# Kernel tuning notes

Measured on AMD Instinct MI355X. Metric: run time of the kernel, lower is better.

The kernel has to match this reference:

```python
import jax, jax.numpy as jnp
import numpy as np

B, N, K = 4096, 87, 87


def setup_inputs() -> dict:
    key = jax.random.key(0)
    ks = jax.random.split(key, 6)
    x = jax.random.normal(ks[0], (B, N, N), dtype=jnp.float32)
    evals = jax.random.uniform(ks[1], (B, K), dtype=jnp.float32)
    evecs = jax.random.normal(ks[2], (B, N, K), dtype=jnp.float32)
    # learned per-node diffusion times (torch inits to 0, clamped to 1e-8;
    # use small positive values to exercise the exp decay)
    diffusion_time = jax.random.uniform(ks[3], (N,), dtype=jnp.float32) * 0.1
    # MiniMLP: single Linear(2*N -> N)
    lim = 1.0 / np.sqrt(2 * N)
    W = jax.random.uniform(ks[4], (N, 2 * N), minval=-lim, maxval=lim, dtype=jnp.float32)
    b = jax.random.uniform(ks[5], (N,), minval=-lim, maxval=lim, dtype=jnp.float32)
    return {"x": x, "evals": evals, "evecs": evecs,
            "diffusion_time": diffusion_time, "W": W, "b": b}


def reference(x, evals, evecs, diffusion_time, W, b):
    # clamp diffusion times (torch does this in-place on .data)
    t = jnp.maximum(diffusion_time, 1e-8)                     # (N,)
    # expa[b,i,m] = exp(-t_i * eval[b,m])
    expa = jnp.exp(-t[None, :, None] * evals[:, None, :])     # (B,N,K)
    # kernel[b,i,j] = sum_m evec[b,i,m] * expa[b,i,m] * evec[b,j,m]
    # (equivalent to the diag_embed + triple matmul + diagonal in the torch code)
    kernel = jnp.einsum('bim,bjm->bij', evecs * expa, evecs)  # (B,N,N)
    x_diffuse = jnp.concatenate([x, kernel], axis=2)          # (B,N,2N)
    return x_diffuse @ W.T + b                                # (B,N,N)
```

## Files before the change

kernel.cpp:

```cpp
#include <hip/hip_runtime.h>
#include <hip/hip_bf16.h>
#include <math.h>

#define NN    87
#define NN2   (NN * NN)
#define EPW   92
#define EFN   8012
#define XSN   8020
#define WPH   104
#define WPANEL (96 * WPH)
#define NT    256

#define WS_W     0
#define WS_EPAD  (2 * WPANEL * 2)
#define EPAD_N   8360
#define WS_NEED  (WS_EPAD + EPAD_N * 4)

typedef __attribute__((ext_vector_type(8))) short bf16x8;
typedef __attribute__((ext_vector_type(4))) short bf16x4;
typedef __attribute__((ext_vector_type(4))) float f32x4;
typedef float f32x4u __attribute__((ext_vector_type(4), aligned(4)));

__device__ __forceinline__ short f2bf(float f) {
    __hip_bfloat16 h = __float2bfloat16(f);
    return *(short*)&h;
}

__device__ __forceinline__ void gl16(const float* g, float* l) {
    __builtin_amdgcn_global_load_lds(
        (const __attribute__((address_space(1))) void*)g,
        (__attribute__((address_space(3))) void*)l, 16, 0, 0);
}

__global__ void prep(const float* __restrict__ W, const float* __restrict__ evecs,
                     int B, char* __restrict__ ws)
{
    int idx = (int)blockIdx.x * NT + (int)threadIdx.x;
    short* wp = (short*)(ws + WS_W);
    float* ep = (float*)(ws + WS_EPAD);
    if (idx < 2 * WPANEL) {
        int p = idx / WPANEL, rem = idx - p * WPANEL;
        int r = rem / WPH, c = rem - r * WPH;
        short v = 0;
        if (r < NN && c < NN) v = f2bf(W[r * (2 * NN) + p * NN + c]);
        wp[idx] = v;
    }
    int i2 = idx - 2 * WPANEL;
    if (i2 >= 0 && i2 < EPAD_N)
        ep[i2] = (i2 < NN2) ? evecs[(size_t)(B - 1) * NN2 + i2] : 0.f;
}

template <bool WS>
__device__ __forceinline__ bf16x8 wload(const short* __restrict__ wp,
                                        const float* __restrict__ gW,
                                        int panel, int jrow, int jcl, int k0, bool tailKs)
{
    if constexpr (WS) {
        return *(const bf16x8*)&wp[panel * WPANEL + jrow * WPH + k0];
    } else {
        float v[8];
        if (!tailKs) {
            f32x4u a  = *(const f32x4u*)(gW + jcl * (2 * NN) + panel * NN + k0);
            f32x4u b4 = *(const f32x4u*)(gW + jcl * (2 * NN) + panel * NN + k0 + 4);
            v[0] = a.x; v[1] = a.y; v[2] = a.z; v[3] = a.w;
            v[4] = b4.x; v[5] = b4.y; v[6] = b4.z; v[7] = b4.w;
        } else {
            #pragma unroll
            for (int q = 0; q < 8; ++q) {
                int k = k0 + q;
                v[q] = (k < NN) ? gW[jcl * (2 * NN) + panel * NN + k] : 0.f;
            }
        }
        bf16x8 o;
        #pragma unroll
        for (int q = 0; q < 8; ++q) o[q] = f2bf(v[q]);
        return o;
    }
}

template <bool WS>
__global__ __launch_bounds__(NT, 4)
void fused(const float* __restrict__ gx, const float* __restrict__ gevals,
           const float* __restrict__ gevecs, const float* __restrict__ dtime,
           const float* __restrict__ gW, const float* __restrict__ bias,
           const char* __restrict__ ws, int B, float* __restrict__ out)
{
    __shared__ __align__(16) float sE[EFN];
    __shared__ __align__(16) short sX[XSN];
    __shared__ float sLam[96];
    short* const sD = (short*)sE;

    const int b    = (int)blockIdx.x;
    const int tid  = (int)threadIdx.x;
    const int lane = tid & 63;
    const int wave = tid >> 6;
    const int l15  = lane & 15;
    const int lk   = lane >> 4;
    const int i0   = (wave >> 1) * 48;
    const int j0   = (wave & 1) * 48;

    const float* __restrict__ Eb = gevecs + (size_t)b * NN2;
    const float* __restrict__ xb = gx     + (size_t)b * NN2;
    const short* wp = nullptr;
    if constexpr (WS) {
        wp = (const short*)(ws + WS_W);
        if (b == B - 1) Eb = (const float*)(ws + WS_EPAD);
    }

    if (tid < 96) sLam[tid] = (tid < NN) ? gevals[(size_t)b * NN + tid] : 3e38f;

    int iw[3], jw[3], iru[3], jru[3];
    float tr_[3];
    #pragma unroll
    for (int r = 0; r < 3; ++r) {
        iw[r]  = i0 + 16 * r + l15;
        jw[r]  = j0 + 16 * r + l15;
        iru[r] = (iw[r] < NN) ? iw[r] : NN - 1;
        jru[r] = (jw[r] < NN) ? jw[r] : NN - 1;
        tr_[r] = fmaxf(dtime[iru[r]], 1e-8f);
    }

    if (tid < 8) sE[NN * EPW + tid] = 0.f;

    if constexpr (WS) {
        for (int vc = wave; vc < 32; vc += 4) {
            int p   = vc * 256 + lane * 4;
            int row = p / EPW;
            int col = p - row * EPW;
            const float* g = Eb + row * NN + col;
            if (vc < 31) gl16(g, &sE[vc * 256]);
            else if (lane < 17) gl16(g, &sE[vc * 256]);
        }
    } else {
        for (int u = tid; u < NN * 22; u += NT) {
            int r = u / 22, sg = u - r * 22, c = sg * 4;
            const float* pE = Eb + r * NN + c;
            if (sg < 21) *(f32x4*)&sE[r * EPW + c] = *(const f32x4u*)pE;
            else { f32x4 t; t.x = pE[0]; t.y = pE[1]; t.z = pE[2]; t.w = 0.f;
                   *(f32x4*)&sE[r * EPW + c] = t; }
        }
        for (int u = tid; u < NN * 4; u += NT) {
            int r = u >> 2, c = 88 + (u & 3);
            sE[r * EPW + c] = 0.f;
        }
    }

    float xq[8][4];
    float x7568 = 0.f;
    #pragma unroll
    for (int k = 0; k < 8; ++k) {
        int u = tid + k * NT;
        int uc = (u < 1892) ? u : 1891;
        f32x4u t = *(const f32x4u*)(xb + 4 * uc);
        xq[k][0] = t.x; xq[k][1] = t.y; xq[k][2] = t.z; xq[k][3] = t.w;
    }
    if (tid == 0) x7568 = xb[7568];

    if constexpr (WS) {
        asm volatile("s_waitcnt vmcnt(8) lgkmcnt(0)" ::: "memory");
        __builtin_amdgcn_s_barrier();
        __builtin_amdgcn_sched_barrier(0);
    } else {
        __syncthreads();
    }

    f32x4 acc1[3][3];
    #pragma unroll
    for (int c = 0; c < 3; ++c)
        #pragma unroll
        for (int r = 0; r < 3; ++r) acc1[c][r] = (f32x4){0.f, 0.f, 0.f, 0.f};

    #pragma unroll
    for (int ks = 0; ks < 3; ++ks) {
        const int k0 = ks * 32 + lk * 8;
        f32x4 la  = *(const f32x4*)&sLam[k0];
        f32x4 lb4 = *(const f32x4*)&sLam[k0 + 4];
        float l8_[8] = {la.x, la.y, la.z, la.w, lb4.x, lb4.y, lb4.z, lb4.w};

        bf16x8 ef[3], af[3];
        #pragma unroll
        for (int c = 0; c < 3; ++c) {
            f32x4 lo = *(const f32x4*)&sE[jru[c] * EPW + k0];
            f32x4 hi = *(const f32x4*)&sE[jru[c] * EPW + k0 + 4];
            #pragma unroll
            for (int q = 0; q < 4; ++q) { ef[c][q] = f2bf(lo[q]); ef[c][q + 4] = f2bf(hi[q]); }
        }
        #pragma unroll
        for (int r = 0; r < 3; ++r) {
            f32x4 lo = *(const f32x4*)&sE[iru[r] * EPW + k0];
            f32x4 hi = *(const f32x4*)&sE[iru[r] * EPW + k0 + 4];
            #pragma unroll
            for (int q = 0; q < 4; ++q) {
                af[r][q]     = f2bf(lo[q] * __expf(-tr_[r] * l8_[q]));
                af[r][q + 4] = f2bf(hi[q] * __expf(-tr_[r] * l8_[q + 4]));
            }
        }
        #pragma unroll
        for (int c = 0; c < 3; ++c)
            #pragma unroll
            for (int r = 0; r < 3; ++r)
                acc1[c][r] = __builtin_amdgcn_mfma_f32_16x16x32_bf16(ef[c], af[r], acc1[c][r], 0, 0, 0);
    }
    __syncthreads();

    #pragma unroll
    for (int c = 0; c < 3; ++c) {
        const int jb = j0 + 16 * c + lk * 4;
        if (jb < EPW) {
            #pragma unroll
            for (int r = 0; r < 3; ++r) {
                if (iw[r] < NN) {
                    bf16x4 v = {f2bf(acc1[c][r][0]), f2bf(acc1[c][r][1]),
                                f2bf(acc1[c][r][2]), f2bf(acc1[c][r][3])};
                    *(bf16x4*)&sD[iw[r] * EPW + jb] = v;
                }
            }
        }
    }
    if (tid < 4) sD[NN * EPW + tid] = 0;
    __builtin_amdgcn_sched_barrier(0);

    #pragma unroll
    for (int k = 0; k < 8; ++k) {
        int u = tid + k * NT;
        if (u < 1892) {
            int f = 4 * u;
            #pragma unroll
            for (int e = 0; e < 4; ++e) {
                int fe = f + e;
                if (fe < NN2) {
                    int r = fe / NN, c = fe - r * NN;
                    sX[r * EPW + c] = f2bf(xq[k][e]);
                }
            }
        }
    }
    if (tid == 0) sX[86 * EPW + 86] = f2bf(x7568);
    for (int u = tid; u < NN * 5; u += NT) {
        int r = u / 5, c = NN + u % 5;
        sX[r * EPW + c] = 0;
    }
    if (tid < 16) sX[NN * EPW + tid] = 0;

    bf16x8 wfx[3][3];
    float bjv[3][4];
    #pragma unroll
    for (int ks = 0; ks < 3; ++ks)
        #pragma unroll
        for (int wr = 0; wr < 3; ++wr)
            wfx[ks][wr] = wload<WS>(wp, gW, 0, jw[wr], jru[wr], ks * 32 + lk * 8, ks == 2);
    #pragma unroll
    for (int wr = 0; wr < 3; ++wr) {
        const int jb = j0 + 16 * wr + lk * 4;
        if (jb + 3 < NN) {
            f32x4u t = *(const f32x4u*)(bias + jb);
            bjv[wr][0] = t.x; bjv[wr][1] = t.y; bjv[wr][2] = t.z; bjv[wr][3] = t.w;
        } else {
            #pragma unroll
            for (int q = 0; q < 4; ++q) bjv[wr][q] = (jb + q < NN) ? bias[jb + q] : 0.f;
        }
    }
    __syncthreads();

    f32x4 acc2[3][3];
    #pragma unroll
    for (int wr = 0; wr < 3; ++wr)
        #pragma unroll
        for (int xc = 0; xc < 3; ++xc) {
            acc2[wr][xc][0] = bjv[wr][0]; acc2[wr][xc][1] = bjv[wr][1];
            acc2[wr][xc][2] = bjv[wr][2]; acc2[wr][xc][3] = bjv[wr][3];
        }

    #pragma unroll
    for (int ks = 0; ks < 3; ++ks) {
        const int k0 = ks * 32 + lk * 8;
        bf16x8 xf[3];
        #pragma unroll
        for (int xc = 0; xc < 3; ++xc) {
            bf16x4 lo = *(const bf16x4*)&sX[iru[xc] * EPW + k0];
            bf16x4 hi = *(const bf16x4*)&sX[iru[xc] * EPW + k0 + 4];
            #pragma unroll
            for (int q = 0; q < 4; ++q) { xf[xc][q] = lo[q]; xf[xc][q + 4] = hi[q]; }
        }
        #pragma unroll
        for (int wr = 0; wr < 3; ++wr)
            #pragma unroll
            for (int xc = 0; xc < 3; ++xc)
                acc2[wr][xc] = __builtin_amdgcn_mfma_f32_16x16x32_bf16(wfx[ks][wr], xf[xc], acc2[wr][xc], 0, 0, 0);
    }
    #pragma unroll
    for (int ks = 0; ks < 3; ++ks) {
        const int k0 = ks * 32 + lk * 8;
        bf16x8 wfd[3], df[3];
        #pragma unroll
        for (int wr = 0; wr < 3; ++wr)
            wfd[wr] = wload<WS>(wp, gW, 1, jw[wr], jru[wr], k0, ks == 2);
        #pragma unroll
        for (int xc = 0; xc < 3; ++xc) {
            bf16x4 lo = *(const bf16x4*)&sD[iru[xc] * EPW + k0];
            bf16x4 hi = *(const bf16x4*)&sD[iru[xc] * EPW + k0 + 4];
            #pragma unroll
            for (int q = 0; q < 4; ++q) { df[xc][q] = lo[q]; df[xc][q + 4] = hi[q]; }
        }
        #pragma unroll
        for (int wr = 0; wr < 3; ++wr)
            #pragma unroll
            for (int xc = 0; xc < 3; ++xc)
                acc2[wr][xc] = __builtin_amdgcn_mfma_f32_16x16x32_bf16(wfd[wr], df[xc], acc2[wr][xc], 0, 0, 0);
    }

    {
        float* __restrict__ gb = out + (size_t)b * NN2;
        #pragma unroll
        for (int wr = 0; wr < 3; ++wr) {
            const int jb = j0 + 16 * wr + lk * 4;
            #pragma unroll
            for (int xc = 0; xc < 3; ++xc) {
                const int i = iw[xc];
                if (i < NN) {
                    if (jb + 3 < NN) {
                        f32x4u v;
                        v.x = acc2[wr][xc][0]; v.y = acc2[wr][xc][1];
                        v.z = acc2[wr][xc][2]; v.w = acc2[wr][xc][3];
                        *(f32x4u*)&gb[i * NN + jb] = v;
                    } else {
                        #pragma unroll
                        for (int q = 0; q < 4; ++q)
                            if (jb + q < NN) gb[i * NN + jb + q] = acc2[wr][xc][q];
                    }
                }
            }
        }
    }
}

extern "C" void kernel_launch(void* const* d_in, const int* in_sizes, int n_in,
                              void* d_out, int out_size, void* d_ws, size_t ws_size,
                              hipStream_t stream)
{
    const float* x     = (const float*)d_in[0];
    const float* evals = (const float*)d_in[1];
    const float* evecs = (const float*)d_in[2];
    const float* dtime = (const float*)d_in[3];
    const float* W     = (const float*)d_in[4];
    const float* bias  = (const float*)d_in[5];
    float* out = (float*)d_out;

    const int B = in_sizes[1] / NN;

    if (ws_size >= (size_t)WS_NEED) {
        const int prep_elems = 2 * WPANEL + EPAD_N;
        prep<<<(prep_elems + NT - 1) / NT, NT, 0, stream>>>(W, evecs, B, (char*)d_ws);
        fused<true><<<dim3(B), dim3(NT), 0, stream>>>(x, evals, evecs, dtime, W, bias,
                                                      (const char*)d_ws, B, out);
    } else {
        fused<false><<<dim3(B), dim3(NT), 0, stream>>>(x, evals, evecs, dtime, W, bias,
                                                       nullptr, B, out);
    }
}
```

Baseline: 96.33 us.

## Make fused kernel persistent and prefetch next batch's evecs during GEMM

Switches to a persistent grid of 768 blocks that loop over batches. While each batch's output GEMM runs, the next batch's evecs are staged into shared memory and its evals are prefetched into a double-buffered array. x is now read straight from global into registers instead of going through shared memory, W fragments are loaded once per iteration, and occupancy drops to 3 blocks per CU. This aims to hide load latency and cut launch and per-block setup costs, at the risk of higher register pressure and less parallelism from the smaller grid.

Result: slower. 158.8 us (+64.9%).

```diff
diff --git a/kernel.cpp b/kernel.cpp
--- a/kernel.cpp
+++ b/kernel.cpp
@@ -5,16 +5,18 @@
 #define NN    87
 #define NN2   (NN * NN)
 #define EPW   92
-#define EFN   8012
-#define XSN   8020
+#define EFN   (NN * EPW + 8)
+#define SDN   (NN * EPW + 4)
 #define WPH   104
 #define WPANEL (96 * WPH)
 #define NT    256
-
+#define GRIDB 768
+
+#define PAD_N    8360
 #define WS_W     0
 #define WS_EPAD  (2 * WPANEL * 2)
-#define EPAD_N   8360
-#define WS_NEED  (WS_EPAD + EPAD_N * 4)
+#define WS_XPAD  (WS_EPAD + PAD_N * 4)
+#define WS_NEED  (WS_XPAD + PAD_N * 4)
 
 typedef __attribute__((ext_vector_type(8))) short bf16x8;
 typedef __attribute__((ext_vector_type(4))) short bf16x4;
@@ -33,21 +35,23 @@
 }
 
 __global__ void prep(const float* __restrict__ W, const float* __restrict__ evecs,
-                     int B, char* __restrict__ ws)
+                     const float* __restrict__ x, int B, char* __restrict__ ws)
 {
     int idx = (int)blockIdx.x * NT + (int)threadIdx.x;
-    short* wp = (short*)(ws + WS_W);
-    float* ep = (float*)(ws + WS_EPAD);
+    short* wpp = (short*)(ws + WS_W);
+    float* ep  = (float*)(ws + WS_EPAD);
+    float* xp  = (float*)(ws + WS_XPAD);
     if (idx < 2 * WPANEL) {
         int p = idx / WPANEL, rem = idx - p * WPANEL;
         int r = rem / WPH, c = rem - r * WPH;
         short v = 0;
         if (r < NN && c < NN) v = f2bf(W[r * (2 * NN) + p * NN + c]);
-        wp[idx] = v;
+        wpp[idx] = v;
     }
     int i2 = idx - 2 * WPANEL;
-    if (i2 >= 0 && i2 < EPAD_N)
-        ep[i2] = (i2 < NN2) ? evecs[(size_t)(B - 1) * NN2 + i2] : 0.f;
+    if (i2 >= 0 && i2 < PAD_N) ep[i2] = (i2 < NN2) ? evecs[(size_t)(B - 1) * NN2 + i2] : 0.f;
+    int i3 = i2 - PAD_N;
+    if (i3 >= 0 && i3 < PAD_N) xp[i3] = (i3 < NN2) ? x[(size_t)(B - 1) * NN2 + i3] : 0.f;
 }
 
 template <bool WS>
@@ -79,18 +83,44 @@
 }
 
 template <bool WS>
-__global__ __launch_bounds__(NT, 4)
+__device__ __forceinline__ void stageE(const float* __restrict__ Eb, float* __restrict__ sE,
+                                       int tid, int wave, int lane)
+{
+    if constexpr (WS) {
+        for (int vc = wave; vc < 32; vc += 4) {
+            int p   = vc * 256 + lane * 4;
+            int row = p / EPW;
+            int col = p - row * EPW;
+            const float* g = Eb + row * NN + col;
+            if (vc < 31) gl16(g, &sE[vc * 256]);
+            else if (lane < 17) gl16(g, &sE[vc * 256]);
+        }
+    } else {
+        for (int u = tid; u < NN * 22; u += NT) {
+            int r = u / 22, sg = u - r * 22, c = sg * 4;
+            const float* pE = Eb + r * NN + c;
+            if (sg < 21) *(f32x4*)&sE[r * EPW + c] = *(const f32x4u*)pE;
+            else { f32x4 t; t.x = pE[0]; t.y = pE[1]; t.z = pE[2]; t.w = 0.f;
+                   *(f32x4*)&sE[r * EPW + c] = t; }
+        }
+        for (int u = tid; u < NN * 4; u += NT) {
+            int r = u >> 2, c = 88 + (u & 3);
+            sE[r * EPW + c] = 0.f;
+        }
+    }
+}
+
+template <bool WS>
+__global__ __launch_bounds__(NT, 3)
 void fused(const float* __restrict__ gx, const float* __restrict__ gevals,
            const float* __restrict__ gevecs, const float* __restrict__ dtime,
            const float* __restrict__ gW, const float* __restrict__ bias,
-           const char* __restrict__ ws, int B, float* __restrict__ out)
+           const char* __restrict__ ws, int B, int gridB, float* __restrict__ out)
 {
     __shared__ __align__(16) float sE[EFN];
-    __shared__ __align__(16) short sX[XSN];
-    __shared__ float sLam[96];
-    short* const sD = (short*)sE;
-
-    const int b    = (int)blockIdx.x;
+    __shared__ __align__(16) short sD[SDN];
+    __shared__ float sLam[2][96];
+
     const int tid  = (int)threadIdx.x;
     const int lane = tid & 63;
     const int wave = tid >> 6;
@@ -99,15 +129,14 @@
     const int i0   = (wave >> 1) * 48;
     const int j0   = (wave & 1) * 48;
 
-    const float* __restrict__ Eb = gevecs + (size_t)b * NN2;
-    const float* __restrict__ xb = gx     + (size_t)b * NN2;
-    const short* wp = nullptr;
+    const short* wp   = nullptr;
+    const float* epad = nullptr;
+    const float* xpad = nullptr;
     if constexpr (WS) {
-        wp = (const short*)(ws + WS_W);
-        if (b == B - 1) Eb = (const float*)(ws + WS_EPAD);
-    }
-
-    if (tid < 96) sLam[tid] = (tid < NN) ? gevals[(size_t)b * NN + tid] : 3e38f;
+        wp   = (const short*)(ws + WS_W);
+        epad = (const float*)(ws + WS_EPAD);
+        xpad = (const float*)(ws + WS_XPAD);
+    }
 
     int iw[3], jw[3], iru[3], jru[3];
     float tr_[3];
@@ -120,135 +149,7 @@
         tr_[r] = fmaxf(dtime[iru[r]], 1e-8f);
     }
 
-    if (tid < 8) sE[NN * EPW + tid] = 0.f;
-
-    if constexpr (WS) {
-        for (int vc = wave; vc < 32; vc += 4) {
-            int p   = vc * 256 + lane * 4;
-            int row = p / EPW;
-            int col = p - row * EPW;
-            const float* g = Eb + row * NN + col;
-            if (vc < 31) gl16(g, &sE[vc * 256]);
-            else if (lane < 17) gl16(g, &sE[vc * 256]);
-        }
-    } else {
-        for (int u = tid; u < NN * 22; u += NT) {
-            int r = u / 22, sg = u - r * 22, c = sg * 4;
-            const float* pE = Eb + r * NN + c;
-            if (sg < 21) *(f32x4*)&sE[r * EPW + c] = *(const f32x4u*)pE;
-            else { f32x4 t; t.x = pE[0]; t.y = pE[1]; t.z = pE[2]; t.w = 0.f;
-                   *(f32x4*)&sE[r * EPW + c] = t; }
-        }
-        for (int u = tid; u < NN * 4; u += NT) {
-            int r = u >> 2, c = 88 + (u & 3);
-            sE[r * EPW + c] = 0.f;
-        }
-    }
-
-    float xq[8][4];
-    float x7568 = 0.f;
-    #pragma unroll
-    for (int k = 0; k < 8; ++k) {
-        int u = tid + k * NT;
-        int uc = (u < 1892) ? u : 1891;
-        f32x4u t = *(const f32x4u*)(xb + 4 * uc);
-        xq[k][0] = t.x; xq[k][1] = t.y; xq[k][2] = t.z; xq[k][3] = t.w;
-    }
-    if (tid == 0) x7568 = xb[7568];
-
-    if constexpr (WS) {
-        asm volatile("s_waitcnt vmcnt(8) lgkmcnt(0)" ::: "memory");
-        __builtin_amdgcn_s_barrier();
-        __builtin_amdgcn_sched_barrier(0);
-    } else {
-        __syncthreads();
-    }
-
-    f32x4 acc1[3][3];
-    #pragma unroll
-    for (int c = 0; c < 3; ++c)
-        #pragma unroll
-        for (int r = 0; r < 3; ++r) acc1[c][r] = (f32x4){0.f, 0.f, 0.f, 0.f};
-
-    #pragma unroll
-    for (int ks = 0; ks < 3; ++ks) {
-        const int k0 = ks * 32 + lk * 8;
-        f32x4 la  = *(const f32x4*)&sLam[k0];
-        f32x4 lb4 = *(const f32x4*)&sLam[k0 + 4];
-        float l8_[8] = {la.x, la.y, la.z, la.w, lb4.x, lb4.y, lb4.z, lb4.w};
-
-        bf16x8 ef[3], af[3];
-        #pragma unroll
-        for (int c = 0; c < 3; ++c) {
-            f32x4 lo = *(const f32x4*)&sE[jru[c] * EPW + k0];
-            f32x4 hi = *(const f32x4*)&sE[jru[c] * EPW + k0 + 4];
-            #pragma unroll
-            for (int q = 0; q < 4; ++q) { ef[c][q] = f2bf(lo[q]); ef[c][q + 4] = f2bf(hi[q]); }
-        }
-        #pragma unroll
-        for (int r = 0; r < 3; ++r) {
-            f32x4 lo = *(const f32x4*)&sE[iru[r] * EPW + k0];
-            f32x4 hi = *(const f32x4*)&sE[iru[r] * EPW + k0 + 4];
-            #pragma unroll
-            for (int q = 0; q < 4; ++q) {
-                af[r][q]     = f2bf(lo[q] * __expf(-tr_[r] * l8_[q]));
-                af[r][q + 4] = f2bf(hi[q] * __expf(-tr_[r] * l8_[q + 4]));
-            }
-        }
-        #pragma unroll
-        for (int c = 0; c < 3; ++c)
-            #pragma unroll
-            for (int r = 0; r < 3; ++r)
-                acc1[c][r] = __builtin_amdgcn_mfma_f32_16x16x32_bf16(ef[c], af[r], acc1[c][r], 0, 0, 0);
-    }
-    __syncthreads();
-
-    #pragma unroll
-    for (int c = 0; c < 3; ++c) {
-        const int jb = j0 + 16 * c + lk * 4;
-        if (jb < EPW) {
-            #pragma unroll
-            for (int r = 0; r < 3; ++r) {
-                if (iw[r] < NN) {
-                    bf16x4 v = {f2bf(acc1[c][r][0]), f2bf(acc1[c][r][1]),
-                                f2bf(acc1[c][r][2]), f2bf(acc1[c][r][3])};
-                    *(bf16x4*)&sD[iw[r] * EPW + jb] = v;
-                }
-            }
-        }
-    }
-    if (tid < 4) sD[NN * EPW + tid] = 0;
-    __builtin_amdgcn_sched_barrier(0);
-
-    #pragma unroll
-    for (int k = 0; k < 8; ++k) {
-        int u = tid + k * NT;
-        if (u < 1892) {
-            int f = 4 * u;
-            #pragma unroll
-            for (int e = 0; e < 4; ++e) {
-                int fe = f + e;
-                if (fe < NN2) {
-                    int r = fe / NN, c = fe - r * NN;
-                    sX[r * EPW + c] = f2bf(xq[k][e]);
-                }
-            }
-        }
-    }
-    if (tid == 0) sX[86 * EPW + 86] = f2bf(x7568);
-    for (int u = tid; u < NN * 5; u += NT) {
-        int r = u / 5, c = NN + u % 5;
-        sX[r * EPW + c] = 0;
-    }
-    if (tid < 16) sX[NN * EPW + tid] = 0;
-
-    bf16x8 wfx[3][3];
     float bjv[3][4];
-    #pragma unroll
-    for (int ks = 0; ks < 3; ++ks)
-        #pragma unroll
-        for (int wr = 0; wr < 3; ++wr)
-            wfx[ks][wr] = wload<WS>(wp, gW, 0, jw[wr], jru[wr], ks * 32 + lk * 8, ks == 2);
     #pragma unroll
     for (int wr = 0; wr < 3; ++wr) {
         const int jb = j0 + 16 * wr + lk * 4;
@@ -260,77 +161,201 @@
             for (int q = 0; q < 4; ++q) bjv[wr][q] = (jb + q < NN) ? bias[jb + q] : 0.f;
         }
     }
+
+    if (tid < 8) sE[NN * EPW + tid] = 0.f;
+    if (tid < 4) sD[NN * EPW + tid] = 0;
+
+    const int b0 = (int)blockIdx.x;
+    {
+        const float* Eb = gevecs + (size_t)b0 * NN2;
+        if (WS && b0 == B - 1) Eb = epad;
+        float lamv = 3e38f;
+        if (tid < NN) lamv = gevals[(size_t)b0 * NN + tid];
+        stageE<WS>(Eb, sE, tid, wave, lane);
+        if (tid < 96) sLam[0][tid] = (tid < NN) ? lamv : 3e38f;
+    }
     __syncthreads();
 
-    f32x4 acc2[3][3];
-    #pragma unroll
-    for (int wr = 0; wr < 3; ++wr)
-        #pragma unroll
-        for (int xc = 0; xc < 3; ++xc) {
-            acc2[wr][xc][0] = bjv[wr][0]; acc2[wr][xc][1] = bjv[wr][1];
-            acc2[wr][xc][2] = bjv[wr][2]; acc2[wr][xc][3] = bjv[wr][3];
-        }
-
-    #pragma unroll
-    for (int ks = 0; ks < 3; ++ks) {
-        const int k0 = ks * 32 + lk * 8;
-        bf16x8 xf[3];
-        #pragma unroll
-        for (int xc = 0; xc < 3; ++xc) {
-            bf16x4 lo = *(const bf16x4*)&sX[iru[xc] * EPW + k0];
-            bf16x4 hi = *(const bf16x4*)&sX[iru[xc] * EPW + k0 + 4];
-            #pragma unroll
-            for (int q = 0; q < 4; ++q) { xf[xc][q] = lo[q]; xf[xc][q + 4] = hi[q]; }
-        }
-        #pragma unroll
-        for (int wr = 0; wr < 3; ++wr)
-            #pragma unroll
-            for (int xc = 0; xc < 3; ++xc)
-                acc2[wr][xc] = __builtin_amdgcn_mfma_f32_16x16x32_bf16(wfx[ks][wr], xf[xc], acc2[wr][xc], 0, 0, 0);
-    }
-    #pragma unroll
-    for (int ks = 0; ks < 3; ++ks) {
-        const int k0 = ks * 32 + lk * 8;
-        bf16x8 wfd[3], df[3];
-        #pragma unroll
-        for (int wr = 0; wr < 3; ++wr)
-            wfd[wr] = wload<WS>(wp, gW, 1, jw[wr], jru[wr], k0, ks == 2);
-        #pragma unroll
-        for (int xc = 0; xc < 3; ++xc) {
-            bf16x4 lo = *(const bf16x4*)&sD[iru[xc] * EPW + k0];
-            bf16x4 hi = *(const bf16x4*)&sD[iru[xc] * EPW + k0 + 4];
-            #pragma unroll
-            for (int q = 0; q < 4; ++q) { df[xc][q] = lo[q]; df[xc][q + 4] = hi[q]; }
-        }
-        #pragma unroll
-        for (int wr = 0; wr < 3; ++wr)
-            #pragma unroll
-            for (int xc = 0; xc < 3; ++xc)
-                acc2[wr][xc] = __builtin_amdgcn_mfma_f32_16x16x32_bf16(wfd[wr], df[xc], acc2[wr][xc], 0, 0, 0);
-    }
-
-    {
-        float* __restrict__ gb = out + (size_t)b * NN2;
-        #pragma unroll
-        for (int wr = 0; wr < 3; ++wr) {
-            const int jb = j0 + 16 * wr + lk * 4;
-            #pragma unroll
-            for (int xc = 0; xc < 3; ++xc) {
-                const int i = iw[xc];
-                if (i < NN) {
-                    if (jb + 3 < NN) {
-                        f32x4u v;
-                        v.x = acc2[wr][xc][0]; v.y = acc2[wr][xc][1];
-                        v.z = acc2[wr][xc][2]; v.w = acc2[wr][xc][3];
-                        *(f32x4u*)&gb[i * NN + jb] = v;
-                    } else {
-                        #pragma unroll
-                        for (int q = 0; q < 4; ++q)
-                            if (jb + q < NN) gb[i * NN + jb + q] = acc2[wr][xc][q];
+    for (int it = 0, b = b0; b < B; ++it, b += gridB) {
+        const int  bn = b + gridB;
+        const bool hn = bn < B;
+        const int  lbuf = it & 1;
+
+        f32x4 acc1[3][3];
+        #pragma unroll
+        for (int c = 0; c < 3; ++c)
+            #pragma unroll
+            for (int r = 0; r < 3; ++r) acc1[c][r] = (f32x4){0.f, 0.f, 0.f, 0.f};
+
+        #pragma unroll
+        for (int ks = 0; ks < 3; ++ks) {
+            const int k0 = ks * 32 + lk * 8;
+            f32x4 la  = *(const f32x4*)&sLam[lbuf][k0];
+            f32x4 lb4 = *(const f32x4*)&sLam[lbuf][k0 + 4];
+            float l8_[8] = {la.x, la.y, la.z, la.w, lb4.x, lb4.y, lb4.z, lb4.w};
+
+            bf16x8 ef[3], af[3];
+            #pragma unroll
+            for (int c = 0; c < 3; ++c) {
+                f32x4 lo = *(const f32x4*)&sE[jru[c] * EPW + k0];
+                f32x4 hi = *(const f32x4*)&sE[jru[c] * EPW + k0 + 4];
+                #pragma unroll
+                for (int q = 0; q < 4; ++q) { ef[c][q] = f2bf(lo[q]); ef[c][q + 4] = f2bf(hi[q]); }
+            }
+            #pragma unroll
+            for (int r = 0; r < 3; ++r) {
+                f32x4 lo = *(const f32x4*)&sE[iru[r] * EPW + k0];
+                f32x4 hi = *(const f32x4*)&sE[iru[r] * EPW + k0 + 4];
+                #pragma unroll
+                for (int q = 0; q < 4; ++q) {
+                    af[r][q]     = f2bf(lo[q] * __expf(-tr_[r] * l8_[q]));
+                    af[r][q + 4] = f2bf(hi[q] * __expf(-tr_[r] * l8_[q + 4]));
+                }
+            }
+            #pragma unroll
+            for (int c = 0; c < 3; ++c)
+                #pragma unroll
+                for (int r = 0; r < 3; ++r)
+                    acc1[c][r] = __builtin_amdgcn_mfma_f32_16x16x32_bf16(ef[c], af[r], acc1[c][r], 0, 0, 0);
+        }
+        __syncthreads();
+
+        #pragma unroll
+        for (int c = 0; c < 3; ++c) {
+            const int jb = j0 + 16 * c + lk * 4;
+            if (jb < EPW) {
+                #pragma unroll
+                for (int r = 0; r < 3; ++r) {
+                    if (iw[r] < NN) {
+                        bf16x4 v = {f2bf(acc1[c][r][0]), f2bf(acc1[c][r][1]),
+                                    f2bf(acc1[c][r][2]), f2bf(acc1[c][r][3])};
+                        *(bf16x4*)&sD[iw[r] * EPW + jb] = v;
                     }
                 }
             }
         }
+
+        bf16x8 wfx[3][3], wfd[3][3];
+        #pragma unroll
+        for (int ks = 0; ks < 3; ++ks)
+            #pragma unroll
+            for (int wr = 0; wr < 3; ++wr) {
+                wfx[ks][wr] = wload<WS>(wp, gW, 0, jw[wr], jru[wr], ks * 32 + lk * 8, ks == 2);
+                wfd[ks][wr] = wload<WS>(wp, gW, 1, jw[wr], jru[wr], ks * 32 + lk * 8, ks == 2);
+            }
+        float lamn = 3e38f;
+        if (hn && tid < NN) lamn = gevals[(size_t)bn * NN + tid];
+
+        const float* xbb = gx + (size_t)b * NN2;
+        bool xvec = true;
+        if (b == B - 1) { if (WS) xbb = xpad; else xvec = false; }
+        float xr[3][3][8];
+        #pragma unroll
+        for (int xc = 0; xc < 3; ++xc)
+            #pragma unroll
+            for (int ks = 0; ks < 3; ++ks) {
+                const int off = iru[xc] * NN + ks * 32 + lk * 8;
+                if (xvec) {
+                    f32x4u a  = *(const f32x4u*)(xbb + off);
+                    f32x4u b4 = *(const f32x4u*)(xbb + off + 4);
+                    xr[xc][ks][0] = a.x;  xr[xc][ks][1] = a.y;
+                    xr[xc][ks][2] = a.z;  xr[xc][ks][3] = a.w;
+                    xr[xc][ks][4] = b4.x; xr[xc][ks][5] = b4.y;
+                    xr[xc][ks][6] = b4.z; xr[xc][ks][7] = b4.w;
+                } else {
+                    #pragma unroll
+                    for (int q = 0; q < 8; ++q) {
+                        int o = off + q;
+                        xr[xc][ks][q] = xbb[(o < NN2) ? o : (NN2 - 1)];
+                    }
+                }
+            }
+
+        __builtin_amdgcn_sched_barrier(0);
+
+        if (hn) {
+            const float* Ebn = gevecs + (size_t)bn * NN2;
+            if (WS && bn == B - 1) Ebn = epad;
+            stageE<WS>(Ebn, sE, tid, wave, lane);
+        }
+
+        asm volatile("s_waitcnt lgkmcnt(0)" ::: "memory");
+        __builtin_amdgcn_s_barrier();
+        __builtin_amdgcn_sched_barrier(0);
+
+        bf16x8 xf[3][3];
+        #pragma unroll
+        for (int xc = 0; xc < 3; ++xc)
+            #pragma unroll
+            for (int ks = 0; ks < 3; ++ks)
+                #pragma unroll
+                for (int q = 0; q < 8; ++q)
+                    xf[xc][ks][q] = f2bf(xr[xc][ks][q]);
+
+        f32x4 acc2[3][3];
+        #pragma unroll
+        for (int wr = 0; wr < 3; ++wr)
+            #pragma unroll
+            for (int xc = 0; xc < 3; ++xc) {
+                acc2[wr][xc][0] = bjv[wr][0]; acc2[wr][xc][1] = bjv[wr][1];
+                acc2[wr][xc][2] = bjv[wr][2]; acc2[wr][xc][3] = bjv[wr][3];
+            }
+
+        #pragma unroll
+        for (int ks = 0; ks < 3; ++ks)
+            #pragma unroll
+            for (int wr = 0; wr < 3; ++wr)
+                #pragma unroll
+                for (int xc = 0; xc < 3; ++xc)
+                    acc2[wr][xc] = __builtin_amdgcn_mfma_f32_16x16x32_bf16(
+                        wfx[ks][wr], xf[xc][ks], acc2[wr][xc], 0, 0, 0);
+
+        #pragma unroll
+        for (int ks = 0; ks < 3; ++ks) {
+            const int k0 = ks * 32 + lk * 8;
+            bf16x8 df[3];
+            #pragma unroll
+            for (int xc = 0; xc < 3; ++xc) {
+                bf16x4 lo = *(const bf16x4*)&sD[iru[xc] * EPW + k0];
+                bf16x4 hi = *(const bf16x4*)&sD[iru[xc] * EPW + k0 + 4];
+                #pragma unroll
+                for (int q = 0; q < 4; ++q) { df[xc][q] = lo[q]; df[xc][q + 4] = hi[q]; }
+            }
+            #pragma unroll
+            for (int wr = 0; wr < 3; ++wr)
+                #pragma unroll
+                for (int xc = 0; xc < 3; ++xc)
+                    acc2[wr][xc] = __builtin_amdgcn_mfma_f32_16x16x32_bf16(
+                        wfd[ks][wr], df[xc], acc2[wr][xc], 0, 0, 0);
+        }
+
+        if (hn && tid < 96) sLam[(it + 1) & 1][tid] = (tid < NN) ? lamn : 3e38f;
+
+        {
+            float* __restrict__ gb = out + (size_t)b * NN2;
+            #pragma unroll
+            for (int wr = 0; wr < 3; ++wr) {
+                const int jb = j0 + 16 * wr + lk * 4;
+                #pragma unroll
+                for (int xc = 0; xc < 3; ++xc) {
+                    const int i = iw[xc];
+                    if (i < NN) {
+                        if (jb + 3 < NN) {
+                            f32x4u v;
+                            v.x = acc2[wr][xc][0]; v.y = acc2[wr][xc][1];
+                            v.z = acc2[wr][xc][2]; v.w = acc2[wr][xc][3];
+                            *(f32x4u*)&gb[i * NN + jb] = v;
+                        } else {
+                            #pragma unroll
+                            for (int q = 0; q < 4; ++q)
+                                if (jb + q < NN) gb[i * NN + jb + q] = acc2[wr][xc][q];
+                        }
+                    }
+                }
+            }
+        }
+
+        if (hn) __syncthreads();
     }
 }
 
@@ -347,14 +372,15 @@
     float* out = (float*)d_out;
 
     const int B = in_sizes[1] / NN;
+    const int gridB = (B < GRIDB) ? B : GRIDB;
 
     if (ws_size >= (size_t)WS_NEED) {
-        const int prep_elems = 2 * WPANEL + EPAD_N;
-        prep<<<(prep_elems + NT - 1) / NT, NT, 0, stream>>>(W, evecs, B, (char*)d_ws);
-        fused<true><<<dim3(B), dim3(NT), 0, stream>>>(x, evals, evecs, dtime, W, bias,
-                                                      (const char*)d_ws, B, out);
+        const int prep_elems = 2 * WPANEL + 2 * PAD_N;
+        prep<<<(prep_elems + NT - 1) / NT, NT, 0, stream>>>(W, evecs, x, B, (char*)d_ws);
+        fused<true><<<dim3(gridB), dim3(NT), 0, stream>>>(x, evals, evecs, dtime, W, bias,
+                                                          (const char*)d_ws, B, gridB, out);
     } else {
-        fused<false><<<dim3(B), dim3(NT), 0, stream>>>(x, evals, evecs, dtime, W, bias,
-                                                       nullptr, B, out);
-    }
-}
+        fused<false><<<dim3(gridB), dim3(NT), 0, stream>>>(x, evals, evecs, dtime, W, bias,
+                                                           nullptr, B, gridB, out);
+    }
+}
```
